# Performance work log

Measured on AMD Instinct MI355X. Metric: run time of the kernel, lower is better.

The kernel has to match this reference:

```python
import jax, jax.numpy as jnp
import numpy as np

EPS = 1e-5

def _conv2d(x, w, b, pad):
    y = jax.lax.conv_general_dilated(x, w, (1, 1), [(pad, pad), (pad, pad)],
                                     dimension_numbers=('NCHW', 'OIHW', 'NCHW'))
    return y + b[None, :, None, None]

def _layernorm2d(x, g, beta):
    # channel-wise LayerNorm per spatial location (LayerNorm2d)
    mu = jnp.mean(x, axis=1, keepdims=True)
    var = jnp.var(x, axis=1, keepdims=True)
    return (x - mu) * jax.lax.rsqrt(var + EPS) * g[None, :, None, None] + beta[None, :, None, None]

def _deform_conv2d(x, offset, w, b, pad):
    # torchvision deform_conv2d semantics (stride 1, dilation 1, 1 group, no mask)
    # x: [B,C,H,W]; offset: [B,2*K*K,H,W] with (dy,dx) per kernel tap; w: [O,C,K,K]
    B, C, H, W = x.shape
    K = w.shape[-1]
    off = offset.reshape(B, K * K, 2, H, W)
    by = jnp.arange(H, dtype=x.dtype)[:, None]   # [H,1]
    bx = jnp.arange(W, dtype=x.dtype)[None, :]   # [1,W]

    def sample(im, py, px):
        # im [C,H,W], py/px [H,W] -> bilinear sample with zero padding outside
        y0 = jnp.floor(py); x0 = jnp.floor(px)
        wy = py - y0; wx = px - x0
        y0i = y0.astype(jnp.int32); x0i = x0.astype(jnp.int32)
        def g(yi, xi):
            valid = (yi >= 0) & (yi < H) & (xi >= 0) & (xi < W)
            v = im[:, jnp.clip(yi, 0, H - 1), jnp.clip(xi, 0, W - 1)]
            return v * valid.astype(im.dtype)
        v00 = g(y0i, x0i);     v01 = g(y0i, x0i + 1)
        v10 = g(y0i + 1, x0i); v11 = g(y0i + 1, x0i + 1)
        return (v00 * (1 - wy) * (1 - wx) + v01 * (1 - wy) * wx
                + v10 * wy * (1 - wx) + v11 * wy * wx)

    vsample = jax.vmap(sample)
    out = jnp.zeros((B, w.shape[0], H, W), dtype=x.dtype)
    for k in range(K * K):  # small fixed tap loop (<=49)
        ki, kj = k // K, k % K
        py = by + (ki - pad) + off[:, k, 0]  # [B,H,W]
        px = bx + (kj - pad) + off[:, k, 1]
        s = vsample(x, py, px)               # [B,C,H,W]
        out = out + jnp.einsum('bchw,oc->bohw', s, w[:, :, ki, kj])
    return out + b[None, :, None, None]


def setup_inputs() -> dict:
    key = jax.random.key(0)
    ks = jax.random.split(key, 12)
    B, C, H, W = 4, 64, 192, 192
    s = 0.02
    inp = {
        'x': jax.random.normal(ks[0], (B, C, H, W), jnp.float32),
        'ln_w': jnp.ones((C,), jnp.float32),
        'ln_b': jnp.zeros((C,), jnp.float32),
        'w_in': jax.random.normal(ks[1], (2 * C, C), jnp.float32) * s,
        'b_in': jnp.zeros((2 * C,), jnp.float32),
        'w_out': jax.random.normal(ks[2], (C, C), jnp.float32) * s,
        'b_out': jnp.zeros((C,), jnp.float32),
        'dw1': jax.random.normal(ks[3], (C, C, 7, 7), jnp.float32) * s,
        'db1': jnp.zeros((C,), jnp.float32),
        'dw2': jax.random.normal(ks[4], (C, C, 5, 5), jnp.float32) * s,
        'db2': jnp.zeros((C,), jnp.float32),
        'dw3': jax.random.normal(ks[5], (C, C, 3, 3), jnp.float32) * s,
        'db3': jnp.zeros((C,), jnp.float32),
        'ow1': jax.random.normal(ks[6], (2 * 7 * 7, C, 5, 5), jnp.float32) * s,
        'ob1': jnp.zeros((2 * 7 * 7,), jnp.float32),
        'ow2': jax.random.normal(ks[7], (2 * 5 * 5, C, 5, 5), jnp.float32) * s,
        'ob2': jnp.zeros((2 * 5 * 5,), jnp.float32),
        'ow3': jax.random.normal(ks[8], (2 * 3 * 3, C, 3, 3), jnp.float32) * s,
        'ob3': jnp.zeros((2 * 3 * 3,), jnp.float32),
    }
    return inp


def reference(x, ln_w, ln_b, w_in, b_in, w_out, b_out,
              dw1, db1, dw2, db2, dw3, db3,
              ow1, ob1, ow2, ob2, ow3, ob3):
    tmp = x
    h = _layernorm2d(x, ln_w, ln_b)
    h = jnp.einsum('bchw,oc->bohw', h, w_in) + b_in[None, :, None, None]  # 1x1 conv_in
    C = x.shape[1]
    x1, x2 = h[:, :C], h[:, C:]
    off = _conv2d(x1, ow1, ob1, 2)
    x1 = _deform_conv2d(x1, off, dw1, db1, 3)
    off = _conv2d(x1, ow2, ob2, 2)
    x1 = _deform_conv2d(x1, off, dw2, db2, 2)
    off = _conv2d(x1, ow3, ob3, 1)
    x1 = _deform_conv2d(x1, off, dw3, db3, 1)
    h = x1 + x2
    h = jnp.einsum('bchw,oc->bohw', h, w_out) + b_out[None, :, None, None]  # 1x1 conv_out
    return h + tmp
```

## Files before the change

### kernel.cpp

```cpp
#include <hip/hip_runtime.h>

#define HH 192
#define WID 192
#define HW (HH*WID)
#define CB 64
#define BB 4
#define NPOS (BB*HW)

typedef __attribute__((ext_vector_type(8))) _Float16 half8v;
typedef __attribute__((ext_vector_type(4))) _Float16 half4v;
typedef __attribute__((ext_vector_type(4))) float f32x4;
typedef __attribute__((ext_vector_type(16))) float f32x16;

static __device__ inline half8v splat8(_Float16 x) {
    half8v v = {x, x, x, x, x, x, x, x};
    return v;
}


template<int KK, int CO, int OP>
__global__ void k_wth(const float* __restrict__ w, _Float16* __restrict__ wt)
{
    int idx = blockIdx.x * 256 + threadIdx.x;
    constexpr int TOT = KK * OP * 64;
    if (idx >= TOT) return;
    int k  = idx / (OP * 64);
    int r  = idx % (OP * 64);
    int cs = r / (OP * 8);
    int r2 = r % (OP * 8);
    int o  = r2 / 8;
    int j  = r2 % 8;
    int c  = cs * 8 + j;
    float v = (o < CO) ? w[((size_t)o * 64 + c) * KK + k] : 0.f;
    wt[idx] = (_Float16)v;
}

__global__ __launch_bounds__(256) void k_lnconv_mfma(
    const float* __restrict__ x, const float* __restrict__ g, const float* __restrict__ be,
    const _Float16* __restrict__ wt_in, const float* __restrict__ b_in,
    _Float16* __restrict__ x1, _Float16* __restrict__ x2)
{
    int p0  = blockIdx.x * 128;
    int b   = p0 / HW;
    int hwb = p0 % HW;

    int lane = threadIdx.x & 63;
    int wave = threadIdx.x >> 6;
    int l31  = lane & 31;
    int h    = lane >> 5;
    int pos  = hwb + wave * 32 + l31;

    const float* xp = x + (size_t)b * CB * HW + pos;

    float v[32];
    float sum = 0.f, sumsq = 0.f;
#pragma unroll
    for (int m = 0; m < 4; m++)
#pragma unroll
        for (int j = 0; j < 8; j++) {
            float t = xp[(size_t)(m * 16 + h * 8 + j) * HW];
            v[m * 8 + j] = t; sum += t; sumsq += t * t;
        }
    sum   += __shfl_xor(sum, 32);
    sumsq += __shfl_xor(sumsq, 32);
    float mu  = sum * (1.f / 64.f);
    float var = sumsq * (1.f / 64.f) - mu * mu;
    float inv = rsqrtf(var + 1e-5f);

    half8v bf[4];
#pragma unroll
    for (int m = 0; m < 4; m++)
#pragma unroll
        for (int j = 0; j < 8; j++) {
            int c = m * 16 + h * 8 + j;
            bf[m][j] = (_Float16)((v[m * 8 + j] - mu) * inv * g[c] + be[c]);
        }

    f32x16 acc[4];
#pragma unroll
    for (int tI = 0; tI < 4; tI++)
#pragma unroll
        for (int r = 0; r < 16; r++) acc[tI][r] = 0.f;

    const half8v* wbase = (const half8v*)wt_in;
#pragma unroll
    for (int m = 0; m < 4; m++) {
        int cs = m * 2 + h;
        const half8v* wp = wbase + (size_t)cs * 128;
#pragma unroll
        for (int tI = 0; tI < 4; tI++) {
            half8v a = wp[tI * 32 + l31];
            acc[tI] = __builtin_amdgcn_mfma_f32_32x32x16_f16(a, bf[m], acc[tI], 0, 0, 0);
        }
    }

    _Float16* o1 = x1 + (size_t)b * HW * 64 + (size_t)pos * 8;
    _Float16* o2 = x2 + (size_t)b * HW * 64 + (size_t)pos * 8;
#pragma unroll
    for (int tI = 0; tI < 4; tI++) {
        _Float16* ob = (tI < 2) ? o1 : o2;
        int obase = (tI & 1) * 32;
#pragma unroll
        for (int gidx = 0; gidx < 4; gidx++) {
            int o = obase + gidx * 8 + 4 * h;
            float4 bb = *(const float4*)&b_in[tI * 32 + gidx * 8 + 4 * h];
            half4v r;
            r[0] = (_Float16)(acc[tI][gidx * 4 + 0] + bb.x);
            r[1] = (_Float16)(acc[tI][gidx * 4 + 1] + bb.y);
            r[2] = (_Float16)(acc[tI][gidx * 4 + 2] + bb.z);
            r[3] = (_Float16)(acc[tI][gidx * 4 + 3] + bb.w);
            *(half4v*)&ob[(size_t)(o >> 3) * HW * 8 + (o & 7)] = r;
        }
    }
}

template<int K, int PAD, int HALO>
__global__ __launch_bounds__(256) void k_sconv(
    const _Float16* __restrict__ xin, const float* __restrict__ offp,
    const _Float16* __restrict__ wtb, const float* __restrict__ bias,
    _Float16* __restrict__ outp)
{
    constexpr int KK = K * K;
    constexpr int RB = 16 + 2 * HALO;
    constexpr int WB = 8  + 2 * HALO;

    __shared__ half8v sm[RB * WB * 8];

    int bi  = blockIdx.x;
    int b   = bi / 288;
    int tt  = bi % 288;
    int by0 = (tt / 24) * 16;
    int bx0 = (tt % 24) * 8;
    int ry0 = by0 - HALO;
    int rx0 = bx0 - HALO;

    const _Float16* xb  = xin + (size_t)b * HW * 64;

    {
        _Float16* smlin = (_Float16*)sm;
        constexpr int CH = RB * WB * 8;
        for (int i0 = 0; i0 < CH; i0 += 256) {
            int i     = i0 + (int)threadIdx.x;
            int wbse  = i0 + ((int)threadIdx.x & 192);
            if (i < CH) {
                int pix = i >> 3;
                int ts  = i & 7;
                int pl  = ts ^ (pix & 7);
                int r   = pix / WB;
                int cc  = pix - r * WB;
                int yr  = min(max(ry0 + r,  0), HH - 1);
                int xc  = min(max(rx0 + cc, 0), WID - 1);
                const _Float16* src = xb + ((size_t)pl * HW + (size_t)(yr * WID + xc)) * 8;
                __builtin_amdgcn_global_load_lds(src, &smlin[(size_t)wbse * 8], 16, 0, 0);
            }
        }
    }
    __syncthreads();

    int t    = threadIdx.x;
    int lane = t & 63;
    int wave = t >> 6;
    int l31  = lane & 31;
    int h    = lane >> 5;
    int prow = l31 >> 3;
    int pcol = l31 & 7;

    int yt = by0 + wave * 4 + prow;
    int xt = bx0 + pcol;
    int gp = b * HW + yt * WID + xt;

    const half8v* wbase = (const half8v*)wtb;

    f32x16 acc0 = {0.f,0.f,0.f,0.f,0.f,0.f,0.f,0.f,0.f,0.f,0.f,0.f,0.f,0.f,0.f,0.f};
    f32x16 acc1 = {0.f,0.f,0.f,0.f,0.f,0.f,0.f,0.f,0.f,0.f,0.f,0.f,0.f,0.f,0.f,0.f};

    const float2* offj = (const float2*)offp + gp;
    float2 offc = offj[0];

    int ki = 0, kj = 0;
    for (int k = 0; k < KK; k++) {
        float2 offn = offj[(size_t)(k + 1) * NPOS];

        half8v a0[4], a1[4];
#pragma unroll
        for (int m = 0; m < 4; m++) {
            int cs = m * 2 + h;
            const half8v* wp = wbase + ((size_t)k * 8 + cs) * 64;
            a0[m] = wp[l31];
            a1[m] = wp[32 + l31];
        }

        float py = (float)(yt + ki - PAD) + offc.x;
        float px = (float)(xt + kj - PAD) + offc.y;
        float fy = floorf(py), fx = floorf(px);
        float wy = py - fy, wx = px - fx;
        int iy0 = (int)fy, ix0 = (int)fx;
        int iy1 = iy0 + 1, ix1 = ix0 + 1;
        float m00 = (iy0 >= 0 && iy0 < HH && ix0 >= 0 && ix0 < WID) ? 1.f : 0.f;
        float m01 = (iy0 >= 0 && iy0 < HH && ix1 >= 0 && ix1 < WID) ? 1.f : 0.f;
        float m10 = (iy1 >= 0 && iy1 < HH && ix0 >= 0 && ix0 < WID) ? 1.f : 0.f;
        float m11 = (iy1 >= 0 && iy1 < HH && ix1 >= 0 && ix1 < WID) ? 1.f : 0.f;
        half8v w00v = splat8((_Float16)((1.f - wy) * (1.f - wx) * m00));
        half8v w01v = splat8((_Float16)((1.f - wy) * wx * m01));
        half8v w10v = splat8((_Float16)(wy * (1.f - wx) * m10));
        half8v w11v = splat8((_Float16)(wy * wx * m11));

        bool fast = (iy0 >= ry0) && (iy1 <= ry0 + RB - 1) &&
                    (ix0 >= rx0) && (ix1 <= rx0 + WB - 1);

        if (__builtin_expect(fast, 1)) {
            int p00 = (iy0 - ry0) * WB + (ix0 - rx0);
            int p01 = p00 + 1, p10 = p00 + WB, p11 = p00 + WB + 1;
            int s00 = p00 & 7, s01 = p01 & 7, s10 = p10 & 7, s11 = p11 & 7;
#pragma unroll
            for (int m = 0; m < 4; m++) {
                int cs = m * 2 + h;
                half8v c00 = sm[p00 * 8 + (cs ^ s00)];
                half8v c01 = sm[p01 * 8 + (cs ^ s01)];
                half8v c10 = sm[p10 * 8 + (cs ^ s10)];
                half8v c11 = sm[p11 * 8 + (cs ^ s11)];
                half8v bf = c00 * w00v + c01 * w01v + c10 * w10v + c11 * w11v;
                acc0 = __builtin_amdgcn_mfma_f32_32x32x16_f16(a0[m], bf, acc0, 0, 0, 0);
                acc1 = __builtin_amdgcn_mfma_f32_32x32x16_f16(a1[m], bf, acc1, 0, 0, 0);
            }
        } else {
            int cy0 = min(max(iy0, 0), HH - 1), cy1 = min(max(iy1, 0), HH - 1);
            int cx0 = min(max(ix0, 0), WID - 1), cx1 = min(max(ix1, 0), WID - 1);
            size_t i00 = (size_t)(cy0 * WID + cx0) * 8, i01 = (size_t)(cy0 * WID + cx1) * 8;
            size_t i10 = (size_t)(cy1 * WID + cx0) * 8, i11 = (size_t)(cy1 * WID + cx1) * 8;
#pragma unroll
            for (int m = 0; m < 4; m++) {
                const _Float16* xq = xb + (size_t)(m * 2 + h) * HW * 8;
                half8v c00 = *(const half8v*)(xq + i00);
                half8v c01 = *(const half8v*)(xq + i01);
                half8v c10 = *(const half8v*)(xq + i10);
                half8v c11 = *(const half8v*)(xq + i11);
                half8v bf = c00 * w00v + c01 * w01v + c10 * w10v + c11 * w11v;
                acc0 = __builtin_amdgcn_mfma_f32_32x32x16_f16(a0[m], bf, acc0, 0, 0, 0);
                acc1 = __builtin_amdgcn_mfma_f32_32x32x16_f16(a1[m], bf, acc1, 0, 0, 0);
            }
        }

        offc = offn;
        kj++;
        if (kj == K) { kj = 0; ki++; }
    }

    int hwp = yt * WID + xt;
    _Float16* ob = outp + (size_t)b * HW * 64 + (size_t)hwp * 8 + 4 * h;
#pragma unroll
    for (int g = 0; g < 4; g++) {
        float4 bb0 = *(const float4*)&bias[g * 8 + 4 * h];
        half4v r0;
        r0[0] = (_Float16)(acc0[g * 4 + 0] + bb0.x);
        r0[1] = (_Float16)(acc0[g * 4 + 1] + bb0.y);
        r0[2] = (_Float16)(acc0[g * 4 + 2] + bb0.z);
        r0[3] = (_Float16)(acc0[g * 4 + 3] + bb0.w);
        *(half4v*)&ob[(size_t)g * HW * 8] = r0;
        float4 bb1 = *(const float4*)&bias[32 + g * 8 + 4 * h];
        half4v r1;
        r1[0] = (_Float16)(acc1[g * 4 + 0] + bb1.x);
        r1[1] = (_Float16)(acc1[g * 4 + 1] + bb1.y);
        r1[2] = (_Float16)(acc1[g * 4 + 2] + bb1.z);
        r1[3] = (_Float16)(acc1[g * 4 + 3] + bb1.w);
        *(half4v*)&ob[(size_t)(4 + g) * HW * 8] = r1;
    }
}

template<int K, int PAD, int CT, int CO>
__global__ __launch_bounds__(256) void k_soconv(
    const _Float16* __restrict__ xin,
    const _Float16* __restrict__ wtb, const float* __restrict__ bias,
    float* __restrict__ outf)
{
    constexpr int KK = K * K;
    constexpr int KTAP = CO / 2;
    constexpr int HALO = PAD;
    constexpr int RB = 16 + 2 * HALO;
    constexpr int WB = 8  + 2 * HALO;
    constexpr int OP = CT * 32;

    __shared__ half8v sm[RB * WB * 8];

    int bi  = blockIdx.x;
    int b   = bi / 288;
    int tt  = bi % 288;
    int by0 = (tt / 24) * 16;
    int bx0 = (tt % 24) * 8;
    int ry0 = by0 - HALO;
    int rx0 = bx0 - HALO;

    const _Float16* xb = xin + (size_t)b * HW * 64;

    {
        _Float16* smlin = (_Float16*)sm;
        constexpr int CH = RB * WB * 8;
        for (int i0 = 0; i0 < CH; i0 += 256) {
            int i    = i0 + (int)threadIdx.x;
            int wbse = i0 + ((int)threadIdx.x & 192);
            if (i < CH) {
                int pix = i >> 3;
                int ts  = i & 7;
                int pl  = ts ^ (pix & 7);
                int r   = pix / WB;
                int cc  = pix - r * WB;
                int yr  = ry0 + r;
                int xc  = rx0 + cc;
                bool ok = (yr >= 0 && yr < HH && xc >= 0 && xc < WID);
                if (ok) {
                    const _Float16* src = xb + ((size_t)pl * HW + (size_t)(yr * WID + xc)) * 8;
                    __builtin_amdgcn_global_load_lds(src, &smlin[(size_t)wbse * 8], 16, 0, 0);
                } else {
                    *(half8v*)&smlin[(size_t)i * 8] = splat8((_Float16)0.f);
                }
            }
        }
    }
    __syncthreads();

    int lane = threadIdx.x & 63;
    int wave = threadIdx.x >> 6;
    int l31  = lane & 31;
    int h    = lane >> 5;
    int prow = l31 >> 3;
    int pcol = l31 & 7;

    int ct = wave % CT;
    int pp = wave / CT;

    int xt = bx0 + pcol;
    int yt[CT], gp[CT];
#pragma unroll
    for (int q = 0; q < CT; q++) {
        int g = pp * CT + q;
        yt[q] = by0 + g * 4 + prow;
        gp[q] = b * HW + yt[q] * WID + xt;
    }

    const half8v* wbase = (const half8v*)wtb;

    f32x16 acc[CT];
#pragma unroll
    for (int q = 0; q < CT; q++)
#pragma unroll
        for (int r = 0; r < 16; r++) acc[q][r] = 0.f;

    int ki = 0, kj = 0;
    for (int k = 0; k < KK; k++) {
        int ccx = (xt + kj - PAD) - rx0;
        int pix[CT];
#pragma unroll
        for (int q = 0; q < CT; q++)
            pix[q] = ((yt[q] + ki - PAD) - ry0) * WB + ccx;

#pragma unroll
        for (int m = 0; m < 4; m++) {
            int cs = m * 2 + h;
            const half8v* wp = wbase + ((size_t)k * 8 + cs) * OP;
            half8v a = wp[ct * 32 + l31];
#pragma unroll
            for (int q = 0; q < CT; q++) {
                half8v bf = sm[pix[q] * 8 + (cs ^ (pix[q] & 7))];
                acc[q] = __builtin_amdgcn_mfma_f32_32x32x16_f16(a, bf, acc[q], 0, 0, 0);
            }
        }

        kj++;
        if (kj == K) { kj = 0; ki++; }
    }

#pragma unroll
    for (int q = 0; q < CT; q++) {
#pragma unroll
        for (int gi = 0; gi < 4; gi++) {
            int obase = ct * 32 + 8 * gi + 4 * h;
#pragma unroll
            for (int pr = 0; pr < 2; pr++) {
                int o  = obase + 2 * pr;
                int t0 = o >> 1;
                if (t0 < KTAP) {
                    float2 r;
                    r.x = acc[q][gi * 4 + 2 * pr]     + bias[o];
                    r.y = acc[q][gi * 4 + 2 * pr + 1] + bias[o + 1];
                    *(float2*)&outf[((size_t)t0 * NPOS + gp[q]) * 2] = r;
                }
            }
        }
    }
}

__global__ __launch_bounds__(256) void k_merge_mfma(
    const _Float16* __restrict__ x1f, const _Float16* __restrict__ x2,
    const float* __restrict__ xin, const _Float16* __restrict__ wt_out,
    const float* __restrict__ b_out, float* __restrict__ out)
{
    int p0  = blockIdx.x * 128;
    int b   = p0 / HW;
    int hwb = p0 % HW;

    int lane = threadIdx.x & 63;
    int wave = threadIdx.x >> 6;
    int l31  = lane & 31;
    int h    = lane >> 5;
    int pos  = hwb + wave * 32 + l31;

    const _Float16* a1 = x1f + (size_t)b * HW * 64 + (size_t)pos * 8;
    const _Float16* a2 = x2  + (size_t)b * HW * 64 + (size_t)pos * 8;

    half8v bf[4];
#pragma unroll
    for (int m = 0; m < 4; m++) {
        int cs = m * 2 + h;
        half8v u1 = *(const half8v*)&a1[(size_t)cs * HW * 8];
        half8v u2 = *(const half8v*)&a2[(size_t)cs * HW * 8];
        bf[m] = u1 + u2;
    }

    f32x16 acc[2];
#pragma unroll
    for (int tI = 0; tI < 2; tI++)
#pragma unroll
        for (int r = 0; r < 16; r++) acc[tI][r] = 0.f;

    const half8v* wbase = (const half8v*)wt_out;
#pragma unroll
    for (int m = 0; m < 4; m++) {
        int cs = m * 2 + h;
        const half8v* wp = wbase + (size_t)cs * 64;
#pragma unroll
        for (int tI = 0; tI < 2; tI++) {
            half8v a = wp[tI * 32 + l31];
            acc[tI] = __builtin_amdgcn_mfma_f32_32x32x16_f16(a, bf[m], acc[tI], 0, 0, 0);
        }
    }

    size_t base = (size_t)b * CB * HW + pos;
#pragma unroll
    for (int tI = 0; tI < 2; tI++) {
#pragma unroll
        for (int gidx = 0; gidx < 4; gidx++) {
            int o0 = tI * 32 + gidx * 8 + 4 * h;
#pragma unroll
            for (int i = 0; i < 4; i++) {
                int o = o0 + i;
                out[base + (size_t)o * HW] =
                    acc[tI][gidx * 4 + i] + b_out[o] + xin[base + (size_t)o * HW];
            }
        }
    }
}

extern "C" void kernel_launch(void* const* d_in, const int* in_sizes, int n_in,
                              void* d_out, int out_size, void* d_ws, size_t ws_size,
                              hipStream_t stream)
{
    const float* x     = (const float*)d_in[0];
    const float* ln_w  = (const float*)d_in[1];
    const float* ln_b  = (const float*)d_in[2];
    const float* w_in  = (const float*)d_in[3];
    const float* b_in  = (const float*)d_in[4];
    const float* w_out = (const float*)d_in[5];
    const float* b_out = (const float*)d_in[6];
    const float* dw1   = (const float*)d_in[7];
    const float* db1   = (const float*)d_in[8];
    const float* dw2   = (const float*)d_in[9];
    const float* db2   = (const float*)d_in[10];
    const float* dw3   = (const float*)d_in[11];
    const float* db3   = (const float*)d_in[12];
    const float* ow1   = (const float*)d_in[13];
    const float* ob1   = (const float*)d_in[14];
    const float* ow2   = (const float*)d_in[15];
    const float* ob2   = (const float*)d_in[16];
    const float* ow3   = (const float*)d_in[17];
    const float* ob3   = (const float*)d_in[18];

    _Float16* x1a = (_Float16*)d_ws;
    _Float16* x1b = x1a + (size_t)NPOS * 64;
    _Float16* x2  = x1b + (size_t)NPOS * 64;
    float* off = (float*)(x2 + (size_t)NPOS * 64);
    _Float16* wtd1 = (_Float16*)(off + (size_t)NPOS * 100);
    _Float16* wtd2 = wtd1 + 49 * 64 * 64;
    _Float16* wtd3 = wtd2 + 25 * 64 * 64;
    _Float16* wto1 = wtd3 +  9 * 64 * 64;
    _Float16* wto2 = wto1 + 25 * 128 * 64;
    _Float16* wto3 = wto2 + 25 * 64 * 64;
    _Float16* wtin = wto3 +  9 * 32 * 64;
    _Float16* wtou = wtin + 128 * 64;

    k_wth<49, 64,  64><<<784, 256, 0, stream>>>(dw1, wtd1);
    k_wth<25, 64,  64><<<400, 256, 0, stream>>>(dw2, wtd2);
    k_wth< 9, 64,  64><<<144, 256, 0, stream>>>(dw3, wtd3);
    k_wth<25, 98, 128><<<800, 256, 0, stream>>>(ow1, wto1);
    k_wth<25, 50,  64><<<400, 256, 0, stream>>>(ow2, wto2);
    k_wth< 9, 18,  32><<< 72, 256, 0, stream>>>(ow3, wto3);
    k_wth< 1, 128, 128><<<32, 256, 0, stream>>>(w_in, wtin);
    k_wth< 1, 64,  64><<<16, 256, 0, stream>>>(w_out, wtou);

    k_lnconv_mfma<<<NPOS / 128, 256, 0, stream>>>(x, ln_w, ln_b, wtin, b_in, x1a, x2);

    k_soconv<5, 2, 4, 98><<<1152, 256, 0, stream>>>(x1a, wto1, ob1, off);
    k_sconv<7, 3, 4><<<1152, 256, 0, stream>>>(x1a, off, wtd1, db1, x1b);
    k_soconv<5, 2, 2, 50><<<1152, 256, 0, stream>>>(x1b, wto2, ob2, off);
    k_sconv<5, 2, 3><<<1152, 256, 0, stream>>>(x1b, off, wtd2, db2, x1a);
    k_soconv<3, 1, 1, 18><<<1152, 256, 0, stream>>>(x1a, wto3, ob3, off);
    k_sconv<3, 1, 2><<<1152, 256, 0, stream>>>(x1a, off, wtd3, db3, x1b);

    k_merge_mfma<<<NPOS / 128, 256, 0, stream>>>(x1b, x2, x, wtou, b_out, (float*)d_out);
}
```

Before: 530.9 us.

## Fuse offset conv into deformable conv, keeping offsets in LDS as fp16

The offset-predicting convolution and the deformable convolution now run in one kernel per stage. The offsets are computed into shared memory as fp16 pairs and read back from there, instead of going through a global fp32 buffer. This removes three kernel launches and the global write and read of the offset tensor, and reuses the staged input tile for both convolutions. In exchange the offsets lose precision, and the larger shared memory footprint may lower occupancy.

```diff
diff --git a/kernel.cpp b/kernel.cpp
--- a/kernel.cpp
+++ b/kernel.cpp
@@ -9,6 +9,7 @@
 
 typedef __attribute__((ext_vector_type(8))) _Float16 half8v;
 typedef __attribute__((ext_vector_type(4))) _Float16 half4v;
+typedef __attribute__((ext_vector_type(2))) _Float16 half2v;
 typedef __attribute__((ext_vector_type(4))) float f32x4;
 typedef __attribute__((ext_vector_type(16))) float f32x16;
 
@@ -114,173 +115,21 @@
     }
 }
 
-template<int K, int PAD, int HALO>
-__global__ __launch_bounds__(256) void k_sconv(
-    const _Float16* __restrict__ xin, const float* __restrict__ offp,
-    const _Float16* __restrict__ wtb, const float* __restrict__ bias,
+template<int KD, int PAD, int HALO, int KO, int PADO, int CT>
+__global__ __launch_bounds__(256) void k_fconv(
+    const _Float16* __restrict__ xin,
+    const _Float16* __restrict__ wto, const float* __restrict__ obias,
+    const _Float16* __restrict__ wtd, const float* __restrict__ dbias,
     _Float16* __restrict__ outp)
 {
-    constexpr int KK = K * K;
-    constexpr int RB = 16 + 2 * HALO;
-    constexpr int WB = 8  + 2 * HALO;
-
-    __shared__ half8v sm[RB * WB * 8];
-
-    int bi  = blockIdx.x;
-    int b   = bi / 288;
-    int tt  = bi % 288;
-    int by0 = (tt / 24) * 16;
-    int bx0 = (tt % 24) * 8;
-    int ry0 = by0 - HALO;
-    int rx0 = bx0 - HALO;
-
-    const _Float16* xb  = xin + (size_t)b * HW * 64;
-
-    {
-        _Float16* smlin = (_Float16*)sm;
-        constexpr int CH = RB * WB * 8;
-        for (int i0 = 0; i0 < CH; i0 += 256) {
-            int i     = i0 + (int)threadIdx.x;
-            int wbse  = i0 + ((int)threadIdx.x & 192);
-            if (i < CH) {
-                int pix = i >> 3;
-                int ts  = i & 7;
-                int pl  = ts ^ (pix & 7);
-                int r   = pix / WB;
-                int cc  = pix - r * WB;
-                int yr  = min(max(ry0 + r,  0), HH - 1);
-                int xc  = min(max(rx0 + cc, 0), WID - 1);
-                const _Float16* src = xb + ((size_t)pl * HW + (size_t)(yr * WID + xc)) * 8;
-                __builtin_amdgcn_global_load_lds(src, &smlin[(size_t)wbse * 8], 16, 0, 0);
-            }
-        }
-    }
-    __syncthreads();
-
-    int t    = threadIdx.x;
-    int lane = t & 63;
-    int wave = t >> 6;
-    int l31  = lane & 31;
-    int h    = lane >> 5;
-    int prow = l31 >> 3;
-    int pcol = l31 & 7;
-
-    int yt = by0 + wave * 4 + prow;
-    int xt = bx0 + pcol;
-    int gp = b * HW + yt * WID + xt;
-
-    const half8v* wbase = (const half8v*)wtb;
-
-    f32x16 acc0 = {0.f,0.f,0.f,0.f,0.f,0.f,0.f,0.f,0.f,0.f,0.f,0.f,0.f,0.f,0.f,0.f};
-    f32x16 acc1 = {0.f,0.f,0.f,0.f,0.f,0.f,0.f,0.f,0.f,0.f,0.f,0.f,0.f,0.f,0.f,0.f};
-
-    const float2* offj = (const float2*)offp + gp;
-    float2 offc = offj[0];
-
-    int ki = 0, kj = 0;
-    for (int k = 0; k < KK; k++) {
-        float2 offn = offj[(size_t)(k + 1) * NPOS];
-
-        half8v a0[4], a1[4];
-#pragma unroll
-        for (int m = 0; m < 4; m++) {
-            int cs = m * 2 + h;
-            const half8v* wp = wbase + ((size_t)k * 8 + cs) * 64;
-            a0[m] = wp[l31];
-            a1[m] = wp[32 + l31];
-        }
-
-        float py = (float)(yt + ki - PAD) + offc.x;
-        float px = (float)(xt + kj - PAD) + offc.y;
-        float fy = floorf(py), fx = floorf(px);
-        float wy = py - fy, wx = px - fx;
-        int iy0 = (int)fy, ix0 = (int)fx;
-        int iy1 = iy0 + 1, ix1 = ix0 + 1;
-        float m00 = (iy0 >= 0 && iy0 < HH && ix0 >= 0 && ix0 < WID) ? 1.f : 0.f;
-        float m01 = (iy0 >= 0 && iy0 < HH && ix1 >= 0 && ix1 < WID) ? 1.f : 0.f;
-        float m10 = (iy1 >= 0 && iy1 < HH && ix0 >= 0 && ix0 < WID) ? 1.f : 0.f;
-        float m11 = (iy1 >= 0 && iy1 < HH && ix1 >= 0 && ix1 < WID) ? 1.f : 0.f;
-        half8v w00v = splat8((_Float16)((1.f - wy) * (1.f - wx) * m00));
-        half8v w01v = splat8((_Float16)((1.f - wy) * wx * m01));
-        half8v w10v = splat8((_Float16)(wy * (1.f - wx) * m10));
-        half8v w11v = splat8((_Float16)(wy * wx * m11));
-
-        bool fast = (iy0 >= ry0) && (iy1 <= ry0 + RB - 1) &&
-                    (ix0 >= rx0) && (ix1 <= rx0 + WB - 1);
-
-        if (__builtin_expect(fast, 1)) {
-            int p00 = (iy0 - ry0) * WB + (ix0 - rx0);
-            int p01 = p00 + 1, p10 = p00 + WB, p11 = p00 + WB + 1;
-            int s00 = p00 & 7, s01 = p01 & 7, s10 = p10 & 7, s11 = p11 & 7;
-#pragma unroll
-            for (int m = 0; m < 4; m++) {
-                int cs = m * 2 + h;
-                half8v c00 = sm[p00 * 8 + (cs ^ s00)];
-                half8v c01 = sm[p01 * 8 + (cs ^ s01)];
-                half8v c10 = sm[p10 * 8 + (cs ^ s10)];
-                half8v c11 = sm[p11 * 8 + (cs ^ s11)];
-                half8v bf = c00 * w00v + c01 * w01v + c10 * w10v + c11 * w11v;
-                acc0 = __builtin_amdgcn_mfma_f32_32x32x16_f16(a0[m], bf, acc0, 0, 0, 0);
-                acc1 = __builtin_amdgcn_mfma_f32_32x32x16_f16(a1[m], bf, acc1, 0, 0, 0);
-            }
-        } else {
-            int cy0 = min(max(iy0, 0), HH - 1), cy1 = min(max(iy1, 0), HH - 1);
-            int cx0 = min(max(ix0, 0), WID - 1), cx1 = min(max(ix1, 0), WID - 1);
-            size_t i00 = (size_t)(cy0 * WID + cx0) * 8, i01 = (size_t)(cy0 * WID + cx1) * 8;
-            size_t i10 = (size_t)(cy1 * WID + cx0) * 8, i11 = (size_t)(cy1 * WID + cx1) * 8;
-#pragma unroll
-            for (int m = 0; m < 4; m++) {
-                const _Float16* xq = xb + (size_t)(m * 2 + h) * HW * 8;
-                half8v c00 = *(const half8v*)(xq + i00);
-                half8v c01 = *(const half8v*)(xq + i01);
-                half8v c10 = *(const half8v*)(xq + i10);
-                half8v c11 = *(const half8v*)(xq + i11);
-                half8v bf = c00 * w00v + c01 * w01v + c10 * w10v + c11 * w11v;
-                acc0 = __builtin_amdgcn_mfma_f32_32x32x16_f16(a0[m], bf, acc0, 0, 0, 0);
-                acc1 = __builtin_amdgcn_mfma_f32_32x32x16_f16(a1[m], bf, acc1, 0, 0, 0);
-            }
-        }
-
-        offc = offn;
-        kj++;
-        if (kj == K) { kj = 0; ki++; }
-    }
-
-    int hwp = yt * WID + xt;
-    _Float16* ob = outp + (size_t)b * HW * 64 + (size_t)hwp * 8 + 4 * h;
-#pragma unroll
-    for (int g = 0; g < 4; g++) {
-        float4 bb0 = *(const float4*)&bias[g * 8 + 4 * h];
-        half4v r0;
-        r0[0] = (_Float16)(acc0[g * 4 + 0] + bb0.x);
-        r0[1] = (_Float16)(acc0[g * 4 + 1] + bb0.y);
-        r0[2] = (_Float16)(acc0[g * 4 + 2] + bb0.z);
-        r0[3] = (_Float16)(acc0[g * 4 + 3] + bb0.w);
-        *(half4v*)&ob[(size_t)g * HW * 8] = r0;
-        float4 bb1 = *(const float4*)&bias[32 + g * 8 + 4 * h];
-        half4v r1;
-        r1[0] = (_Float16)(acc1[g * 4 + 0] + bb1.x);
-        r1[1] = (_Float16)(acc1[g * 4 + 1] + bb1.y);
-        r1[2] = (_Float16)(acc1[g * 4 + 2] + bb1.z);
-        r1[3] = (_Float16)(acc1[g * 4 + 3] + bb1.w);
-        *(half4v*)&ob[(size_t)(4 + g) * HW * 8] = r1;
-    }
-}
-
-template<int K, int PAD, int CT, int CO>
-__global__ __launch_bounds__(256) void k_soconv(
-    const _Float16* __restrict__ xin,
-    const _Float16* __restrict__ wtb, const float* __restrict__ bias,
-    float* __restrict__ outf)
-{
-    constexpr int KK = K * K;
-    constexpr int KTAP = CO / 2;
-    constexpr int HALO = PAD;
+    constexpr int KKD = KD * KD;
+    constexpr int KKO = KO * KO;
     constexpr int RB = 16 + 2 * HALO;
     constexpr int WB = 8  + 2 * HALO;
     constexpr int OP = CT * 32;
 
     __shared__ half8v sm[RB * WB * 8];
+    __shared__ unsigned int offs[KKD * 128];
 
     int bi  = blockIdx.x;
     int b   = bi / 288;
@@ -324,68 +173,169 @@
     int h    = lane >> 5;
     int prow = l31 >> 3;
     int pcol = l31 & 7;
-
-    int ct = wave % CT;
-    int pp = wave / CT;
-
-    int xt = bx0 + pcol;
-    int yt[CT], gp[CT];
-#pragma unroll
-    for (int q = 0; q < CT; q++) {
-        int g = pp * CT + q;
-        yt[q] = by0 + g * 4 + prow;
-        gp[q] = b * HW + yt[q] * WID + xt;
-    }
-
-    const half8v* wbase = (const half8v*)wtb;
-
-    f32x16 acc[CT];
-#pragma unroll
-    for (int q = 0; q < CT; q++)
-#pragma unroll
-        for (int r = 0; r < 16; r++) acc[q][r] = 0.f;
+    int xt   = bx0 + pcol;
+
+    {
+        int ct = wave % CT;
+        int pp = wave / CT;
+
+        int ytA[CT], pA[CT];
+#pragma unroll
+        for (int q = 0; q < CT; q++) {
+            int g = pp * CT + q;
+            ytA[q] = by0 + g * 4 + prow;
+            pA[q]  = g * 32 + l31;
+        }
+
+        const half8v* wbase = (const half8v*)wto;
+
+        f32x16 accO[CT];
+#pragma unroll
+        for (int q = 0; q < CT; q++)
+#pragma unroll
+            for (int r = 0; r < 16; r++) accO[q][r] = 0.f;
+
+        int ki = 0, kj = 0;
+        for (int k = 0; k < KKO; k++) {
+            int ccx = (xt + kj - PADO) - rx0;
+            int pixA[CT];
+#pragma unroll
+            for (int q = 0; q < CT; q++)
+                pixA[q] = ((ytA[q] + ki - PADO) - ry0) * WB + ccx;
+
+#pragma unroll
+            for (int m = 0; m < 4; m++) {
+                int cs = m * 2 + h;
+                const half8v* wp = wbase + ((size_t)k * 8 + cs) * OP;
+                half8v a = wp[ct * 32 + l31];
+#pragma unroll
+                for (int q = 0; q < CT; q++) {
+                    half8v bf = sm[pixA[q] * 8 + (cs ^ (pixA[q] & 7))];
+                    accO[q] = __builtin_amdgcn_mfma_f32_32x32x16_f16(a, bf, accO[q], 0, 0, 0);
+                }
+            }
+
+            kj++;
+            if (kj == KO) { kj = 0; ki++; }
+        }
+
+#pragma unroll
+        for (int q = 0; q < CT; q++) {
+#pragma unroll
+            for (int gi = 0; gi < 4; gi++) {
+                int obase = ct * 32 + 8 * gi + 4 * h;
+#pragma unroll
+                for (int pr = 0; pr < 2; pr++) {
+                    int o  = obase + 2 * pr;
+                    int kt = o >> 1;
+                    if (kt < KKD) {
+                        half2v hv;
+                        hv[0] = (_Float16)(accO[q][gi * 4 + 2 * pr]     + obias[o]);
+                        hv[1] = (_Float16)(accO[q][gi * 4 + 2 * pr + 1] + obias[o + 1]);
+                        *(half2v*)&offs[kt * 128 + pA[q]] = hv;
+                    }
+                }
+            }
+        }
+    }
+    __syncthreads();
+
+    int yt   = by0 + wave * 4 + prow;
+    int p128 = wave * 32 + l31;
+
+    const half8v* wbase = (const half8v*)wtd;
+
+    f32x16 acc0 = {0.f,0.f,0.f,0.f,0.f,0.f,0.f,0.f,0.f,0.f,0.f,0.f,0.f,0.f,0.f,0.f};
+    f32x16 acc1 = {0.f,0.f,0.f,0.f,0.f,0.f,0.f,0.f,0.f,0.f,0.f,0.f,0.f,0.f,0.f,0.f};
 
     int ki = 0, kj = 0;
-    for (int k = 0; k < KK; k++) {
-        int ccx = (xt + kj - PAD) - rx0;
-        int pix[CT];
-#pragma unroll
-        for (int q = 0; q < CT; q++)
-            pix[q] = ((yt[q] + ki - PAD) - ry0) * WB + ccx;
-
+    for (int k = 0; k < KKD; k++) {
+        half2v ov = *(const half2v*)&offs[k * 128 + p128];
+        float ox = (float)ov[0];
+        float oy = (float)ov[1];
+
+        half8v a0[4], a1[4];
 #pragma unroll
         for (int m = 0; m < 4; m++) {
             int cs = m * 2 + h;
-            const half8v* wp = wbase + ((size_t)k * 8 + cs) * OP;
-            half8v a = wp[ct * 32 + l31];
-#pragma unroll
-            for (int q = 0; q < CT; q++) {
-                half8v bf = sm[pix[q] * 8 + (cs ^ (pix[q] & 7))];
-                acc[q] = __builtin_amdgcn_mfma_f32_32x32x16_f16(a, bf, acc[q], 0, 0, 0);
+            const half8v* wp = wbase + ((size_t)k * 8 + cs) * 64;
+            a0[m] = wp[l31];
+            a1[m] = wp[32 + l31];
+        }
+
+        float py = (float)(yt + ki - PAD) + ox;
+        float px = (float)(xt + kj - PAD) + oy;
+        float fy = floorf(py), fx = floorf(px);
+        float wy = py - fy, wx = px - fx;
+        int iy0 = (int)fy, ix0 = (int)fx;
+        int iy1 = iy0 + 1, ix1 = ix0 + 1;
+        float m00 = (iy0 >= 0 && iy0 < HH && ix0 >= 0 && ix0 < WID) ? 1.f : 0.f;
+        float m01 = (iy0 >= 0 && iy0 < HH && ix1 >= 0 && ix1 < WID) ? 1.f : 0.f;
+        float m10 = (iy1 >= 0 && iy1 < HH && ix0 >= 0 && ix0 < WID) ? 1.f : 0.f;
+        float m11 = (iy1 >= 0 && iy1 < HH && ix1 >= 0 && ix1 < WID) ? 1.f : 0.f;
+        half8v w00v = splat8((_Float16)((1.f - wy) * (1.f - wx) * m00));
+        half8v w01v = splat8((_Float16)((1.f - wy) * wx * m01));
+        half8v w10v = splat8((_Float16)(wy * (1.f - wx) * m10));
+        half8v w11v = splat8((_Float16)(wy * wx * m11));
+
+        bool fast = (iy0 >= ry0) && (iy1 <= ry0 + RB - 1) &&
+                    (ix0 >= rx0) && (ix1 <= rx0 + WB - 1);
+
+        if (__builtin_expect(fast, 1)) {
+            int p00 = (iy0 - ry0) * WB + (ix0 - rx0);
+            int p01 = p00 + 1, p10 = p00 + WB, p11 = p00 + WB + 1;
+            int s00 = p00 & 7, s01 = p01 & 7, s10 = p10 & 7, s11 = p11 & 7;
+#pragma unroll
+            for (int m = 0; m < 4; m++) {
+                int cs = m * 2 + h;
+                half8v c00 = sm[p00 * 8 + (cs ^ s00)];
+                half8v c01 = sm[p01 * 8 + (cs ^ s01)];
+                half8v c10 = sm[p10 * 8 + (cs ^ s10)];
+                half8v c11 = sm[p11 * 8 + (cs ^ s11)];
+                half8v bf = c00 * w00v + c01 * w01v + c10 * w10v + c11 * w11v;
+                acc0 = __builtin_amdgcn_mfma_f32_32x32x16_f16(a0[m], bf, acc0, 0, 0, 0);
+                acc1 = __builtin_amdgcn_mfma_f32_32x32x16_f16(a1[m], bf, acc1, 0, 0, 0);
+            }
+        } else {
+            int cy0 = min(max(iy0, 0), HH - 1), cy1 = min(max(iy1, 0), HH - 1);
+            int cx0 = min(max(ix0, 0), WID - 1), cx1 = min(max(ix1, 0), WID - 1);
+            size_t i00 = (size_t)(cy0 * WID + cx0) * 8, i01 = (size_t)(cy0 * WID + cx1) * 8;
+            size_t i10 = (size_t)(cy1 * WID + cx0) * 8, i11 = (size_t)(cy1 * WID + cx1) * 8;
+#pragma unroll
+            for (int m = 0; m < 4; m++) {
+                const _Float16* xq = xb + (size_t)(m * 2 + h) * HW * 8;
+                half8v c00 = *(const half8v*)(xq + i00);
+                half8v c01 = *(const half8v*)(xq + i01);
+                half8v c10 = *(const half8v*)(xq + i10);
+                half8v c11 = *(const half8v*)(xq + i11);
+                half8v bf = c00 * w00v + c01 * w01v + c10 * w10v + c11 * w11v;
+                acc0 = __builtin_amdgcn_mfma_f32_32x32x16_f16(a0[m], bf, acc0, 0, 0, 0);
+                acc1 = __builtin_amdgcn_mfma_f32_32x32x16_f16(a1[m], bf, acc1, 0, 0, 0);
             }
         }
 
         kj++;
-        if (kj == K) { kj = 0; ki++; }
-    }
-
-#pragma unroll
-    for (int q = 0; q < CT; q++) {
-#pragma unroll
-        for (int gi = 0; gi < 4; gi++) {
-            int obase = ct * 32 + 8 * gi + 4 * h;
-#pragma unroll
-            for (int pr = 0; pr < 2; pr++) {
-                int o  = obase + 2 * pr;
-                int t0 = o >> 1;
-                if (t0 < KTAP) {
-                    float2 r;
-                    r.x = acc[q][gi * 4 + 2 * pr]     + bias[o];
-                    r.y = acc[q][gi * 4 + 2 * pr + 1] + bias[o + 1];
-                    *(float2*)&outf[((size_t)t0 * NPOS + gp[q]) * 2] = r;
-                }
-            }
-        }
+        if (kj == KD) { kj = 0; ki++; }
+    }
+
+    int hwp = yt * WID + xt;
+    _Float16* ob = outp + (size_t)b * HW * 64 + (size_t)hwp * 8 + 4 * h;
+#pragma unroll
+    for (int g = 0; g < 4; g++) {
+        float4 bb0 = *(const float4*)&dbias[g * 8 + 4 * h];
+        half4v r0;
+        r0[0] = (_Float16)(acc0[g * 4 + 0] + bb0.x);
+        r0[1] = (_Float16)(acc0[g * 4 + 1] + bb0.y);
+        r0[2] = (_Float16)(acc0[g * 4 + 2] + bb0.z);
+        r0[3] = (_Float16)(acc0[g * 4 + 3] + bb0.w);
+        *(half4v*)&ob[(size_t)g * HW * 8] = r0;
+        float4 bb1 = *(const float4*)&dbias[32 + g * 8 + 4 * h];
+        half4v r1;
+        r1[0] = (_Float16)(acc1[g * 4 + 0] + bb1.x);
+        r1[1] = (_Float16)(acc1[g * 4 + 1] + bb1.y);
+        r1[2] = (_Float16)(acc1[g * 4 + 2] + bb1.z);
+        r1[3] = (_Float16)(acc1[g * 4 + 3] + bb1.w);
+        *(half4v*)&ob[(size_t)(4 + g) * HW * 8] = r1;
     }
 }
 
@@ -498,12 +448,9 @@
 
     k_lnconv_mfma<<<NPOS / 128, 256, 0, stream>>>(x, ln_w, ln_b, wtin, b_in, x1a, x2);
 
-    k_soconv<5, 2, 4, 98><<<1152, 256, 0, stream>>>(x1a, wto1, ob1, off);
-    k_sconv<7, 3, 4><<<1152, 256, 0, stream>>>(x1a, off, wtd1, db1, x1b);
-    k_soconv<5, 2, 2, 50><<<1152, 256, 0, stream>>>(x1b, wto2, ob2, off);
-    k_sconv<5, 2, 3><<<1152, 256, 0, stream>>>(x1b, off, wtd2, db2, x1a);
-    k_soconv<3, 1, 1, 18><<<1152, 256, 0, stream>>>(x1a, wto3, ob3, off);
-    k_sconv<3, 1, 2><<<1152, 256, 0, stream>>>(x1a, off, wtd3, db3, x1b);
+    k_fconv<7, 3, 4, 5, 2, 4><<<1152, 256, 0, stream>>>(x1a, wto1, ob1, wtd1, db1, x1b);
+    k_fconv<5, 2, 3, 5, 2, 2><<<1152, 256, 0, stream>>>(x1b, wto2, ob2, wtd2, db2, x1a);
+    k_fconv<3, 1, 2, 3, 1, 1><<<1152, 256, 0, stream>>>(x1a, wto3, ob3, wtd3, db3, x1b);
 
     k_merge_mfma<<<NPOS / 128, 256, 0, stream>>>(x1b, x2, x, wtou, b_out, (float*)d_out);
 }
```

Result: faster. 489.1 us (-7.9%).
